# Kernel optimization log

Hardware: AMD Instinct MI355X
Metric: run time of the kernel (lower is better)

## Reference

```python
import jax, jax.numpy as jnp
import numpy as np

N = 50000        # nodes
E = 800000       # edges (avg degree 16)
C_PREV = 256
HID = 256        # C * 4, C = 64
ALPHA = 0.1      # GCNII-style initial-residual weight
LAMBDA = 0.5     # identity-mapping hyperparameter
LAYER = 1
BN_EPS = 1e-5
GIN_EPS = 0.0    # GIN epsilon (default 0)


def setup_inputs() -> dict:
    key = jax.random.key(0)
    ks = jax.random.split(key, 6)
    s0 = jax.random.normal(ks[0], (N, C_PREV), jnp.float32)
    s1 = jax.random.normal(ks[1], (N, C_PREV), jnp.float32)
    x_0 = jax.random.normal(ks[2], (N, HID), jnp.float32)
    # preprocess MLP: Linear(C_prev -> 4C, bias=False) + BatchNorm + ReLU
    W_pre = jax.random.normal(ks[3], (C_PREV, HID), jnp.float32) / np.sqrt(C_PREV).astype(np.float32)
    gamma = jnp.ones((HID,), jnp.float32)
    beta_bn = jnp.zeros((HID,), jnp.float32)
    # ginii op weight (identity-mapped linear, GCNII style)
    W_op = jax.random.normal(ks[4], (HID, HID), jnp.float32) / np.sqrt(HID).astype(np.float32)
    edge_index = jax.random.randint(ks[5], (2, E), 0, N, dtype=jnp.int32)
    return {"s0": s0, "s1": s1, "x_0": x_0, "W_pre": W_pre, "gamma": gamma,
            "beta_bn": beta_bn, "W_op": W_op, "edge_index": edge_index,
            "drop_prob": 0, "training": 0}


def reference(s0, s1, x_0, W_pre, gamma, beta_bn, W_op, edge_index, drop_prob, training):
    # preprocess1: Linear (no bias) -> BatchNorm (batch stats) -> ReLU
    h = s1 @ W_pre                                        # [N, HID]
    mu = h.mean(axis=0)
    var = h.var(axis=0)
    h = (h - mu) * jax.lax.rsqrt(var + BN_EPS) * gamma + beta_bn
    h = jax.nn.relu(h)

    # ginii: GIN-style sum aggregation over edge_index with initial residual
    # and identity-mapped weight (GCNII trick).
    src, dst = edge_index[0], edge_index[1]
    agg = jax.ops.segment_sum(h[src], dst, num_segments=N)   # [N, HID]
    h = (1.0 + GIN_EPS) * h + agg
    support = (1.0 - ALPHA) * h + ALPHA * x_0
    beta = float(np.log(LAMBDA / LAYER + 1.0))
    out = jax.nn.relu((1.0 - beta) * support + beta * (support @ W_op))
    return out
```

## Files before the change

kernel.cpp:

```cpp
#include <hip/hip_runtime.h>

#define NNODES 50000
#define NEDGES 800000
#define HIDDIM 256
#define NCHUNK  1563
#define GEMMB   256
#define DEGCAP  64
#define EPB     3125
#define NCOARSE 196
#define CCAP    4864
#define NROWS   50176

constexpr float kAlpha = 0.1f;
constexpr float kBnEps = 1e-5f;
constexpr float kBeta  = 0.40546510810816438198f;

typedef __attribute__((ext_vector_type(8))) short  bf16x8;
typedef __attribute__((ext_vector_type(4))) float  f32x4;

typedef __attribute__((address_space(1))) const unsigned int gu32;
typedef __attribute__((address_space(3))) unsigned int       lu32;

static __device__ __forceinline__ unsigned short f2bf(float f) {
  unsigned u = __float_as_uint(f);
  u = (u + 0x7FFFu + ((u >> 16) & 1u)) >> 16;
  return (unsigned short)u;
}
static __device__ __forceinline__ float bf2f(unsigned short h) {
  return __uint_as_float(((unsigned)h) << 16);
}

__global__ __launch_bounds__(256) void prep_t_k(const float* __restrict__ W_pre,
                                                const float* __restrict__ W_op,
                                                unsigned short* __restrict__ wpre_t,
                                                unsigned short* __restrict__ wop_t) {
  __shared__ unsigned short tile[64][66];
  const int b = blockIdx.x;
  const float* W = (b < 16) ? W_pre : W_op;
  unsigned short* Wt = (b < 16) ? wpre_t : wop_t;
  const int tb = b & 15;
  const int k0 = (tb >> 2) * 64, n0 = (tb & 3) * 64;
  const int t = threadIdx.x;
#pragma unroll
  for (int i = 0; i < 16; ++i) {
    int e = i * 256 + t;
    int k = e >> 6, n = e & 63;
    tile[k][n] = f2bf(W[(size_t)(k0 + k) * 256 + n0 + n]);
  }
  __syncthreads();
#pragma unroll
  for (int i = 0; i < 16; ++i) {
    int e = i * 256 + t;
    int n = e >> 6, k = e & 63;
    Wt[(size_t)(n0 + n) * 256 + k0 + k] = tile[k][n];
  }
}

__global__ __launch_bounds__(256) void binA_k(const int* __restrict__ ei,
                                              int* __restrict__ gcnt,
                                              unsigned* __restrict__ coarse) {
  __shared__ int lcnt[NCOARSE];
  __shared__ int loff[NCOARSE];
  __shared__ int lcur[NCOARSE];
  __shared__ int gbase[NCOARSE];
  __shared__ int sc[256];
  __shared__ unsigned buf[EPB];
  const int t = threadIdx.x;
  const int e0 = (int)blockIdx.x * EPB;

  for (int i = t; i < NCOARSE; i += 256) lcnt[i] = 0;
  __syncthreads();
  for (int j = t; j < EPB; j += 256) {
    int d = ei[NEDGES + e0 + j];
    atomicAdd(&lcnt[d >> 8], 1);
  }
  __syncthreads();
  sc[t] = (t < NCOARSE) ? lcnt[t] : 0;
  __syncthreads();
  for (int o = 1; o < 256; o <<= 1) {
    int x = (t >= o) ? sc[t - o] : 0;
    __syncthreads();
    sc[t] += x;
    __syncthreads();
  }
  if (t < NCOARSE) {
    int ex = sc[t] - lcnt[t];
    loff[t] = ex;
    lcur[t] = ex;
    gbase[t] = (lcnt[t] > 0) ? atomicAdd(&gcnt[t], lcnt[t]) : 0;
  }
  __syncthreads();
  for (int j = t; j < EPB; j += 256) {
    int s = ei[e0 + j];
    int d = ei[NEDGES + e0 + j];
    int bk = d >> 8;
    int p = atomicAdd(&lcur[bk], 1);
    buf[p] = ((unsigned)bk << 24) | ((unsigned)(d & 255) << 16) | (unsigned)s;
  }
  __syncthreads();
  for (int i = t; i < EPB; i += 256) {
    unsigned v = buf[i];
    int bk = v >> 24;
    int idx = gbase[bk] + (i - loff[bk]);
    if (idx < CCAP) coarse[(size_t)bk * CCAP + idx] = v;
  }
}

__global__ __launch_bounds__(256) void binB_k(const int* __restrict__ gcnt,
                                              const unsigned* __restrict__ coarse,
                                              unsigned short* __restrict__ esrc16,
                                              int* __restrict__ deg) {
  __shared__ unsigned short els[256 * DEGCAP];
  __shared__ int bcnt[256];
  const int g = blockIdx.x;
  const int t = threadIdx.x;
  bcnt[t] = 0;
  __syncthreads();
  int n = gcnt[g]; if (n > CCAP) n = CCAP;
  for (int i = t; i < n; i += 256) {
    unsigned v = coarse[(size_t)g * CCAP + i];
    int dl = (v >> 16) & 255;
    int p = atomicAdd(&bcnt[dl], 1);
    if (p < DEGCAP) els[dl * DEGCAP + p] = (unsigned short)(v & 0xFFFFu);
  }
  __syncthreads();
  {
    int node = g * 256 + t;
    if (node < NNODES) {
      int dgg = bcnt[t]; if (dgg > DEGCAP) dgg = DEGCAP;
      deg[node] = dgg;
    }
  }
  ushort4* gdst = (ushort4*)(esrc16 + (size_t)g * 256 * DEGCAP);
  const ushort4* lsrc = (const ushort4*)els;
#pragma unroll
  for (int q = 0; q < 16; ++q)
    gdst[q * 256 + t] = lsrc[q * 256 + t];
}

__global__ __launch_bounds__(512) void gemm1_persist_k(
    const float* __restrict__ Ain,
    const unsigned short* __restrict__ Bt,
    unsigned short* __restrict__ Cout,
    float* __restrict__ colsum,
    float* __restrict__ colsumsq,
    int M) {
  __shared__ __align__(16) unsigned short Bl[256 * 256];
  __shared__ __align__(16) unsigned short Al[2][32 * 256];

  const int t    = threadIdx.x;
  const int lane = t & 63;
  const int wid  = t >> 6;
  const int wr   = wid >> 2;
  const int wc   = wid & 3;

  {
    const int lrow = lane >> 5;
    const int lchk = lane & 31;
#pragma unroll
    for (int c = 0; c < 16; ++c) {
      int issue = wid * 16 + c;
      int row = issue * 2 + lrow;
      int srcoff = (lchk * 16) ^ ((row & 7) << 4);
      const char* g = (const char*)Bt + (size_t)row * 512 + srcoff;
      char* l = (char*)Bl + issue * 1024 + lane * 16;
      __builtin_amdgcn_global_load_lds((gu32*)g, (lu32*)l, 16, 0, 0);
    }
  }

  float spart[4] = {0.f, 0.f, 0.f, 0.f};
  float qpart[4] = {0.f, 0.f, 0.f, 0.f};

  auto stageA = [&](int buf, int chunk) {
    const int r0 = chunk * 32;
#pragma unroll
    for (int s = 0; s < 4; ++s) {
      int e   = s * 512 + t;
      int row = e >> 6;
      int c4  = e & 63;
      int arow = r0 + row;
      float4 p = make_float4(0.f, 0.f, 0.f, 0.f);
      if (arow < M) p = *(const float4*)(Ain + (size_t)arow * 256 + c4 * 4);
      short4 v;
      v.x = (short)f2bf(p.x); v.y = (short)f2bf(p.y);
      v.z = (short)f2bf(p.z); v.w = (short)f2bf(p.w);
      char* base = (char*)&Al[buf][0] + row * 512;
      *(short4*)(base + ((c4 * 8) ^ ((row & 7) << 4))) = v;
    }
  };

  stageA(0, blockIdx.x);
  __syncthreads();

  int nc = 0;
  for (int c = blockIdx.x; c < NCHUNK; c += GEMMB, ++nc) {
    const int cur = nc & 1;
    const int cn = c + GEMMB;
    if (cn < NCHUNK) stageA(cur ^ 1, cn);

    f32x4 acc[4] = {};
    const int arow_f = wr * 16 + (lane & 15);
    const int asw = (arow_f & 7) << 4;
#pragma unroll
    for (int ks = 0; ks < 8; ++ks) {
      const int koff = ks * 64 + ((lane >> 4) * 16);
      bf16x8 af = *(const bf16x8*)((char*)&Al[cur][0] + arow_f * 512 + (koff ^ asw));
#pragma unroll
      for (int n = 0; n < 4; ++n) {
        int nr = wc * 64 + n * 16 + (lane & 15);
        bf16x8 bfr = *(const bf16x8*)((char*)Bl + (size_t)nr * 512 + (koff ^ ((nr & 7) << 4)));
        acc[n] = __builtin_amdgcn_mfma_f32_16x16x32_bf16(af, bfr, acc[n], 0, 0, 0);
      }
    }

#pragma unroll
    for (int n = 0; n < 4; ++n) {
      int col = wc * 64 + n * 16 + (lane & 15);
      float s = 0.f, q = 0.f;
#pragma unroll
      for (int r = 0; r < 4; ++r) {
        int row = c * 32 + wr * 16 + (lane >> 4) * 4 + r;
        float v = acc[n][r];
        s += v; q += v * v;
        if (row < M) Cout[(size_t)row * 256 + col] = f2bf(v);
      }
      spart[n] += s; qpart[n] += q;
    }
    __syncthreads();
  }

#pragma unroll
  for (int n = 0; n < 4; ++n) {
    float s = spart[n], q = qpart[n];
    s += __shfl_xor(s, 16); s += __shfl_xor(s, 32);
    q += __shfl_xor(q, 16); q += __shfl_xor(q, 32);
    if (lane < 16) {
      int col = wc * 64 + n * 16 + lane;
      atomicAdd(&colsum[col], s);
      atomicAdd(&colsumsq[col], q);
    }
  }
}

__global__ __launch_bounds__(512) void gemm2_persist_k(
    const unsigned short* __restrict__ Ain,
    const unsigned short* __restrict__ Bt,
    float* __restrict__ Cout,
    int M) {
  __shared__ __align__(16) unsigned short Bl[256 * 256];
  __shared__ __align__(16) unsigned short Al[2][32 * 256];

  const int t    = threadIdx.x;
  const int lane = t & 63;
  const int wid  = t >> 6;
  const int wr   = wid >> 2;
  const int wc   = wid & 3;

  {
    const int lrow = lane >> 5;
    const int lchk = lane & 31;
#pragma unroll
    for (int c = 0; c < 16; ++c) {
      int issue = wid * 16 + c;
      int row = issue * 2 + lrow;
      int srcoff = (lchk * 16) ^ ((row & 7) << 4);
      const char* g = (const char*)Bt + (size_t)row * 512 + srcoff;
      char* l = (char*)Bl + issue * 1024 + lane * 16;
      __builtin_amdgcn_global_load_lds((gu32*)g, (lu32*)l, 16, 0, 0);
    }
  }

  auto stageA = [&](int buf, int chunk) {
    const int lrow = lane >> 5, lchk = lane & 31;
#pragma unroll
    for (int c = 0; c < 2; ++c) {
      int issue = wid * 2 + c;
      int row = issue * 2 + lrow;
      int srcoff = (lchk * 16) ^ ((row & 7) << 4);
      const char* g = (const char*)Ain + (size_t)(chunk * 32 + row) * 512 + srcoff;
      char* l = (char*)&Al[buf][0] + issue * 1024 + lane * 16;
      __builtin_amdgcn_global_load_lds((gu32*)g, (lu32*)l, 16, 0, 0);
    }
  };

  stageA(0, blockIdx.x);
  __syncthreads();

  int nc = 0;
  for (int c = blockIdx.x; c < NCHUNK; c += GEMMB, ++nc) {
    const int cur = nc & 1;
    if (c + GEMMB < NCHUNK) stageA(cur ^ 1, c + GEMMB);

    f32x4 acc[4] = {};
    const int arow_f = wr * 16 + (lane & 15);
    const int asw = (arow_f & 7) << 4;
#pragma unroll
    for (int ks = 0; ks < 8; ++ks) {
      const int koff = ks * 64 + ((lane >> 4) * 16);
      bf16x8 af = *(const bf16x8*)((char*)&Al[cur][0] + arow_f * 512 + (koff ^ asw));
#pragma unroll
      for (int n = 0; n < 4; ++n) {
        int nr = wc * 64 + n * 16 + (lane & 15);
        bf16x8 bfr = *(const bf16x8*)((char*)Bl + (size_t)nr * 512 + (koff ^ ((nr & 7) << 4)));
        acc[n] = __builtin_amdgcn_mfma_f32_16x16x32_bf16(af, bfr, acc[n], 0, 0, 0);
      }
    }

#pragma unroll
    for (int n = 0; n < 4; ++n) {
      int col = wc * 64 + n * 16 + (lane & 15);
#pragma unroll
      for (int r = 0; r < 4; ++r) {
        int rl = wr * 16 + (lane >> 4) * 4 + r;
        int row = c * 32 + rl;
        if (row < M) {
          unsigned short sv = *(const unsigned short*)
              ((char*)&Al[cur][0] + rl * 512 + ((col * 2) ^ ((rl & 7) << 4)));
          Cout[(size_t)row * 256 + col] =
              fmaxf((1.f - kBeta) * bf2f(sv) + kBeta * acc[n][r], 0.f);
        }
      }
    }
    __syncthreads();
  }
}

__global__ __launch_bounds__(256) void agg_bn_support_k(
    const unsigned short* __restrict__ hb,
    const int* __restrict__ deg,
    const unsigned short* __restrict__ esrc16,
    const float* __restrict__ x0,
    const float* __restrict__ colsum,
    const float* __restrict__ colsumsq,
    const float* __restrict__ gamma,
    const float* __restrict__ beta_bn,
    unsigned short* __restrict__ supp_bf) {
  __shared__ float s_sc[256], s_sh[256];
  {
    int j = threadIdx.x;
    float inv_n = 1.0f / (float)NNODES;
    float mu  = colsum[j] * inv_n;
    float var = colsumsq[j] * inv_n - mu * mu;
    float rstd = rsqrtf(var + kBnEps);
    float g = gamma[j] * rstd;
    s_sc[j] = g;
    s_sh[j] = beta_bn[j] - mu * g;
  }
  __syncthreads();

  const int hw   = threadIdx.x >> 5;
  const int lane = threadIdx.x & 31;
  const int d    = blockIdx.x * 8 + hw;
  const int off  = lane * 8;

  float sc[8], sh[8];
  *(float4*)&sc[0] = *(const float4*)(s_sc + off);
  *(float4*)&sc[4] = *(const float4*)(s_sc + off + 4);
  *(float4*)&sh[0] = *(const float4*)(s_sh + off);
  *(float4*)&sh[4] = *(const float4*)(s_sh + off + 4);

  const int beg = d * DEGCAP;
  int dg = deg[d]; if (dg > DEGCAP) dg = DEGCAP;
  const int end = beg + dg;
  float acc[8] = {0.f, 0.f, 0.f, 0.f, 0.f, 0.f, 0.f, 0.f};

  for (int bb = beg; bb < end; bb += 32) {
    int c32 = end - bb; if (c32 > 32) c32 = 32;
    int myi = esrc16[bb + ((lane < c32) ? lane : 0)];
    int u = 0;
    for (; u + 3 < c32; u += 4) {
      int s0 = __shfl(myi, u, 32),     s1 = __shfl(myi, u + 1, 32);
      int s2 = __shfl(myi, u + 2, 32), s3 = __shfl(myi, u + 3, 32);
      bf16x8 v0 = *(const bf16x8*)(hb + (size_t)s0 * HIDDIM + off);
      bf16x8 v1 = *(const bf16x8*)(hb + (size_t)s1 * HIDDIM + off);
      bf16x8 v2 = *(const bf16x8*)(hb + (size_t)s2 * HIDDIM + off);
      bf16x8 v3 = *(const bf16x8*)(hb + (size_t)s3 * HIDDIM + off);
#pragma unroll
      for (int j = 0; j < 8; ++j) {
        acc[j] += fmaxf(fmaf(bf2f((unsigned short)v0[j]), sc[j], sh[j]), 0.f)
                + fmaxf(fmaf(bf2f((unsigned short)v1[j]), sc[j], sh[j]), 0.f)
                + fmaxf(fmaf(bf2f((unsigned short)v2[j]), sc[j], sh[j]), 0.f)
                + fmaxf(fmaf(bf2f((unsigned short)v3[j]), sc[j], sh[j]), 0.f);
      }
    }
    for (; u < c32; ++u) {
      int s0 = __shfl(myi, u, 32);
      bf16x8 v0 = *(const bf16x8*)(hb + (size_t)s0 * HIDDIM + off);
#pragma unroll
      for (int j = 0; j < 8; ++j)
        acc[j] += fmaxf(fmaf(bf2f((unsigned short)v0[j]), sc[j], sh[j]), 0.f);
    }
  }

  bf16x8 vd = *(const bf16x8*)(hb + (size_t)d * HIDDIM + off);
  f32x4 xa = __builtin_nontemporal_load((const f32x4*)(x0 + (size_t)d * HIDDIM + off));
  f32x4 xb = __builtin_nontemporal_load((const f32x4*)(x0 + (size_t)d * HIDDIM + off + 4));
  float xs[8] = {xa.x, xa.y, xa.z, xa.w, xb.x, xb.y, xb.z, xb.w};
  bf16x8 o;
#pragma unroll
  for (int j = 0; j < 8; ++j) {
    float hv = fmaxf(fmaf(bf2f((unsigned short)vd[j]), sc[j], sh[j]), 0.f);
    o[j] = (short)f2bf((1.f - kAlpha) * (hv + acc[j]) + kAlpha * xs[j]);
  }
  __builtin_nontemporal_store(o, (bf16x8*)(supp_bf + (size_t)d * HIDDIM + off));
}

extern "C" void kernel_launch(void* const* d_in, const int* in_sizes, int n_in,
                              void* d_out, int out_size, void* d_ws, size_t ws_size,
                              hipStream_t stream) {
  const float* s1    = (const float*)d_in[1];
  const float* x0    = (const float*)d_in[2];
  const float* W_pre = (const float*)d_in[3];
  const float* gamma = (const float*)d_in[4];
  const float* betab = (const float*)d_in[5];
  const float* W_op  = (const float*)d_in[6];
  const int*   ei    = (const int*)d_in[7];
  float* out = (float*)d_out;

  const size_t NH = (size_t)NNODES * HIDDIM;
  unsigned short* hbf   = (unsigned short*)d_ws;
  unsigned short* supbf = hbf + NH;
  int*   gcnt     = (int*)(supbf + NH);
  float* colsum   = (float*)(gcnt + NCOARSE);
  float* colsumsq = colsum + HIDDIM;
  unsigned short* wpre_t = (unsigned short*)(colsumsq + HIDDIM);
  unsigned short* wop_t  = wpre_t + 65536;
  int*   deg      = (int*)(wop_t + 65536);
  unsigned short* esrc16 = (unsigned short*)(deg + NROWS);
  unsigned* coarse = (unsigned*)(esrc16 + (size_t)NROWS * DEGCAP);

  hipMemsetAsync(gcnt, 0, (NCOARSE + 2 * HIDDIM) * sizeof(int), stream);

  prep_t_k<<<32, 256, 0, stream>>>(W_pre, W_op, wpre_t, wop_t);

  binA_k<<<256, 256, 0, stream>>>(ei, gcnt, coarse);
  binB_k<<<NCOARSE, 256, 0, stream>>>(gcnt, coarse, esrc16, deg);

  gemm1_persist_k<<<GEMMB, 512, 0, stream>>>(s1, wpre_t, hbf, colsum, colsumsq, NNODES);

  agg_bn_support_k<<<(NNODES + 7) / 8, 256, 0, stream>>>(hbf, deg, esrc16, x0,
                                                         colsum, colsumsq, gamma, betab,
                                                         supbf);

  gemm2_persist_k<<<GEMMB, 512, 0, stream>>>(supbf, wop_t, out, NNODES);
}
```

Measured before the change: 175.3 us.

## Fuse coarse edge binning and x_0 bf16 conversion into persistent GEMM1

Merges the first edge-binning pass into the persistent GEMM1 kernel, reusing the A-tile LDS as scratch while the weight tile loads asynchronously, which removes one launch. The GEMM loop also converts x_0 to bf16 in slices over its first six iterations, so the aggregation kernel reads half as many bytes for the residual term. This costs an extra fp32 read and bf16 write of x_0 inside GEMM1 and adds bf16 rounding error on the residual input.

```diff
diff --git a/kernel.cpp b/kernel.cpp
--- a/kernel.cpp
+++ b/kernel.cpp
@@ -10,6 +10,8 @@
 #define NCOARSE 196
 #define CCAP    4864
 #define NROWS   50176
+#define X8PB    6250
+#define X8PC    1042
 
 constexpr float kAlpha = 0.1f;
 constexpr float kBnEps = 1e-5f;
@@ -56,94 +58,17 @@
   }
 }
 
-__global__ __launch_bounds__(256) void binA_k(const int* __restrict__ ei,
-                                              int* __restrict__ gcnt,
-                                              unsigned* __restrict__ coarse) {
-  __shared__ int lcnt[NCOARSE];
-  __shared__ int loff[NCOARSE];
-  __shared__ int lcur[NCOARSE];
-  __shared__ int gbase[NCOARSE];
-  __shared__ int sc[256];
-  __shared__ unsigned buf[EPB];
-  const int t = threadIdx.x;
-  const int e0 = (int)blockIdx.x * EPB;
-
-  for (int i = t; i < NCOARSE; i += 256) lcnt[i] = 0;
-  __syncthreads();
-  for (int j = t; j < EPB; j += 256) {
-    int d = ei[NEDGES + e0 + j];
-    atomicAdd(&lcnt[d >> 8], 1);
-  }
-  __syncthreads();
-  sc[t] = (t < NCOARSE) ? lcnt[t] : 0;
-  __syncthreads();
-  for (int o = 1; o < 256; o <<= 1) {
-    int x = (t >= o) ? sc[t - o] : 0;
-    __syncthreads();
-    sc[t] += x;
-    __syncthreads();
-  }
-  if (t < NCOARSE) {
-    int ex = sc[t] - lcnt[t];
-    loff[t] = ex;
-    lcur[t] = ex;
-    gbase[t] = (lcnt[t] > 0) ? atomicAdd(&gcnt[t], lcnt[t]) : 0;
-  }
-  __syncthreads();
-  for (int j = t; j < EPB; j += 256) {
-    int s = ei[e0 + j];
-    int d = ei[NEDGES + e0 + j];
-    int bk = d >> 8;
-    int p = atomicAdd(&lcur[bk], 1);
-    buf[p] = ((unsigned)bk << 24) | ((unsigned)(d & 255) << 16) | (unsigned)s;
-  }
-  __syncthreads();
-  for (int i = t; i < EPB; i += 256) {
-    unsigned v = buf[i];
-    int bk = v >> 24;
-    int idx = gbase[bk] + (i - loff[bk]);
-    if (idx < CCAP) coarse[(size_t)bk * CCAP + idx] = v;
-  }
-}
-
-__global__ __launch_bounds__(256) void binB_k(const int* __restrict__ gcnt,
-                                              const unsigned* __restrict__ coarse,
-                                              unsigned short* __restrict__ esrc16,
-                                              int* __restrict__ deg) {
-  __shared__ unsigned short els[256 * DEGCAP];
-  __shared__ int bcnt[256];
-  const int g = blockIdx.x;
-  const int t = threadIdx.x;
-  bcnt[t] = 0;
-  __syncthreads();
-  int n = gcnt[g]; if (n > CCAP) n = CCAP;
-  for (int i = t; i < n; i += 256) {
-    unsigned v = coarse[(size_t)g * CCAP + i];
-    int dl = (v >> 16) & 255;
-    int p = atomicAdd(&bcnt[dl], 1);
-    if (p < DEGCAP) els[dl * DEGCAP + p] = (unsigned short)(v & 0xFFFFu);
-  }
-  __syncthreads();
-  {
-    int node = g * 256 + t;
-    if (node < NNODES) {
-      int dgg = bcnt[t]; if (dgg > DEGCAP) dgg = DEGCAP;
-      deg[node] = dgg;
-    }
-  }
-  ushort4* gdst = (ushort4*)(esrc16 + (size_t)g * 256 * DEGCAP);
-  const ushort4* lsrc = (const ushort4*)els;
-#pragma unroll
-  for (int q = 0; q < 16; ++q)
-    gdst[q * 256 + t] = lsrc[q * 256 + t];
-}
-
-__global__ __launch_bounds__(512) void gemm1_persist_k(
+__global__ __launch_bounds__(512) void gemm1_bin_persist_k(
     const float* __restrict__ Ain,
     const unsigned short* __restrict__ Bt,
     unsigned short* __restrict__ Cout,
     float* __restrict__ colsum,
     float* __restrict__ colsumsq,
+    const int* __restrict__ ei,
+    int* __restrict__ gcnt,
+    unsigned* __restrict__ coarse,
+    const float* __restrict__ x0,
+    unsigned short* __restrict__ x0b,
     int M) {
   __shared__ __align__(16) unsigned short Bl[256 * 256];
   __shared__ __align__(16) unsigned short Al[2][32 * 256];
@@ -166,6 +91,54 @@
       char* l = (char*)Bl + issue * 1024 + lane * 16;
       __builtin_amdgcn_global_load_lds((gu32*)g, (lu32*)l, 16, 0, 0);
     }
+  }
+
+  {
+    int* lcnt  = (int*)&Al[0][0];
+    int* lsum  = lcnt + 256;
+    int* loff  = lsum + 256;
+    int* lcur  = loff + 256;
+    int* gbase = lcur + 256;
+    unsigned* buf = (unsigned*)(gbase + 256);
+
+    if (t < 256) lcnt[t] = 0;
+    __syncthreads();
+    const int e0 = (int)blockIdx.x * EPB;
+    for (int j = t; j < EPB; j += 512) {
+      int d = ei[NEDGES + e0 + j];
+      atomicAdd(&lcnt[d >> 8], 1);
+    }
+    __syncthreads();
+    if (t < 256) lsum[t] = (t < NCOARSE) ? lcnt[t] : 0;
+    __syncthreads();
+    for (int o = 1; o < 256; o <<= 1) {
+      int x = (t < 256 && t >= o) ? lsum[t - o] : 0;
+      __syncthreads();
+      if (t < 256) lsum[t] += x;
+      __syncthreads();
+    }
+    if (t < NCOARSE) {
+      int ex = lsum[t] - lcnt[t];
+      loff[t] = ex;
+      lcur[t] = ex;
+      gbase[t] = (lcnt[t] > 0) ? atomicAdd(&gcnt[t], lcnt[t]) : 0;
+    }
+    __syncthreads();
+    for (int j = t; j < EPB; j += 512) {
+      int s = ei[e0 + j];
+      int d = ei[NEDGES + e0 + j];
+      int bk = d >> 8;
+      int p = atomicAdd(&lcur[bk], 1);
+      buf[p] = ((unsigned)bk << 24) | ((unsigned)(d & 255) << 16) | (unsigned)s;
+    }
+    __syncthreads();
+    for (int i = t; i < EPB; i += 512) {
+      unsigned v = buf[i];
+      int bk = v >> 24;
+      int idx = gbase[bk] + (i - loff[bk]);
+      if (idx < CCAP) coarse[(size_t)bk * CCAP + idx] = v;
+    }
+    __syncthreads();
   }
 
   float spart[4] = {0.f, 0.f, 0.f, 0.f};
@@ -198,6 +171,23 @@
     const int cn = c + GEMMB;
     if (cn < NCHUNK) stageA(cur ^ 1, cn);
 
+    if (nc < 6) {
+      int sub = nc * X8PC;
+      int len = X8PB - sub; if (len > X8PC) len = X8PC;
+      for (int j = t; j < len; j += 512) {
+        int p8 = (int)blockIdx.x * X8PB + sub + j;
+        const float* xp = x0 + (size_t)p8 * 8;
+        float4 a = *(const float4*)xp;
+        float4 cc = *(const float4*)(xp + 4);
+        bf16x8 v;
+        v[0] = (short)f2bf(a.x);  v[1] = (short)f2bf(a.y);
+        v[2] = (short)f2bf(a.z);  v[3] = (short)f2bf(a.w);
+        v[4] = (short)f2bf(cc.x); v[5] = (short)f2bf(cc.y);
+        v[6] = (short)f2bf(cc.z); v[7] = (short)f2bf(cc.w);
+        *(bf16x8*)(x0b + (size_t)p8 * 8) = v;
+      }
+    }
+
     f32x4 acc[4] = {};
     const int arow_f = wr * 16 + (lane & 15);
     const int asw = (arow_f & 7) << 4;
@@ -240,6 +230,38 @@
       atomicAdd(&colsumsq[col], q);
     }
   }
+}
+
+__global__ __launch_bounds__(256) void binB_k(const int* __restrict__ gcnt,
+                                              const unsigned* __restrict__ coarse,
+                                              unsigned short* __restrict__ esrc16,
+                                              int* __restrict__ deg) {
+  __shared__ unsigned short els[256 * DEGCAP];
+  __shared__ int bcnt[256];
+  const int g = blockIdx.x;
+  const int t = threadIdx.x;
+  bcnt[t] = 0;
+  __syncthreads();
+  int n = gcnt[g]; if (n > CCAP) n = CCAP;
+  for (int i = t; i < n; i += 256) {
+    unsigned v = coarse[(size_t)g * CCAP + i];
+    int dl = (v >> 16) & 255;
+    int p = atomicAdd(&bcnt[dl], 1);
+    if (p < DEGCAP) els[dl * DEGCAP + p] = (unsigned short)(v & 0xFFFFu);
+  }
+  __syncthreads();
+  {
+    int node = g * 256 + t;
+    if (node < NNODES) {
+      int dgg = bcnt[t]; if (dgg > DEGCAP) dgg = DEGCAP;
+      deg[node] = dgg;
+    }
+  }
+  ushort4* gdst = (ushort4*)(esrc16 + (size_t)g * 256 * DEGCAP);
+  const ushort4* lsrc = (const ushort4*)els;
+#pragma unroll
+  for (int q = 0; q < 16; ++q)
+    gdst[q * 256 + t] = lsrc[q * 256 + t];
 }
 
 __global__ __launch_bounds__(512) void gemm2_persist_k(
@@ -329,7 +351,7 @@
     const unsigned short* __restrict__ hb,
     const int* __restrict__ deg,
     const unsigned short* __restrict__ esrc16,
-    const float* __restrict__ x0,
+    const unsigned short* __restrict__ x0b,
     const float* __restrict__ colsum,
     const float* __restrict__ colsumsq,
     const float* __restrict__ gamma,
@@ -393,14 +415,12 @@
   }
 
   bf16x8 vd = *(const bf16x8*)(hb + (size_t)d * HIDDIM + off);
-  f32x4 xa = __builtin_nontemporal_load((const f32x4*)(x0 + (size_t)d * HIDDIM + off));
-  f32x4 xb = __builtin_nontemporal_load((const f32x4*)(x0 + (size_t)d * HIDDIM + off + 4));
-  float xs[8] = {xa.x, xa.y, xa.z, xa.w, xb.x, xb.y, xb.z, xb.w};
+  bf16x8 xv = *(const bf16x8*)(x0b + (size_t)d * HIDDIM + off);
   bf16x8 o;
 #pragma unroll
   for (int j = 0; j < 8; ++j) {
     float hv = fmaxf(fmaf(bf2f((unsigned short)vd[j]), sc[j], sh[j]), 0.f);
-    o[j] = (short)f2bf((1.f - kAlpha) * (hv + acc[j]) + kAlpha * xs[j]);
+    o[j] = (short)f2bf((1.f - kAlpha) * (hv + acc[j]) + kAlpha * bf2f((unsigned short)xv[j]));
   }
   __builtin_nontemporal_store(o, (bf16x8*)(supp_bf + (size_t)d * HIDDIM + off));
 }
@@ -420,7 +440,8 @@
   const size_t NH = (size_t)NNODES * HIDDIM;
   unsigned short* hbf   = (unsigned short*)d_ws;
   unsigned short* supbf = hbf + NH;
-  int*   gcnt     = (int*)(supbf + NH);
+  unsigned short* x0b   = supbf + NH;
+  int*   gcnt     = (int*)(x0b + NH);
   float* colsum   = (float*)(gcnt + NCOARSE);
   float* colsumsq = colsum + HIDDIM;
   unsigned short* wpre_t = (unsigned short*)(colsumsq + HIDDIM);
@@ -433,12 +454,12 @@
 
   prep_t_k<<<32, 256, 0, stream>>>(W_pre, W_op, wpre_t, wop_t);
 
-  binA_k<<<256, 256, 0, stream>>>(ei, gcnt, coarse);
+  gemm1_bin_persist_k<<<GEMMB, 512, 0, stream>>>(s1, wpre_t, hbf, colsum, colsumsq,
+                                                 ei, gcnt, coarse, x0, x0b, NNODES);
+
   binB_k<<<NCOARSE, 256, 0, stream>>>(gcnt, coarse, esrc16, deg);
 
-  gemm1_persist_k<<<GEMMB, 512, 0, stream>>>(s1, wpre_t, hbf, colsum, colsumsq, NNODES);
-
-  agg_bn_support_k<<<(NNODES + 7) / 8, 256, 0, stream>>>(hbf, deg, esrc16, x0,
+  agg_bn_support_k<<<(NNODES + 7) / 8, 256, 0, stream>>>(hbf, deg, esrc16, x0b,
                                                          colsum, colsumsq, gamma, betab,
                                                          supbf);
 
```

Measured after the change: 170.5 us. 2.7% less time.
